# Performance work log

Measured on AMD Instinct MI355X. Metric: run time of the kernel, lower is better.

Reference implementation:

```python
import jax, jax.numpy as jnp
import numpy as np

D_MODEL = 1024
NUM_HEADS = 16
D_HEAD = D_MODEL // NUM_HEADS


def setup_inputs() -> dict:
    key = jax.random.key(0)
    ks = jax.random.split(key, 5)
    b, n = 4, 2048
    x = jax.random.normal(ks[0], (b, n, D_MODEL), dtype=jnp.float32)
    s = 1.0 / np.sqrt(D_MODEL)
    w_qkv = jax.random.normal(ks[1], (D_MODEL, 3 * D_MODEL), dtype=jnp.float32) * s
    b_qkv = jax.random.normal(ks[2], (3 * D_MODEL,), dtype=jnp.float32) * 0.01
    w_out = jax.random.normal(ks[3], (D_MODEL, D_MODEL), dtype=jnp.float32) * s
    b_out = jax.random.normal(ks[4], (D_MODEL,), dtype=jnp.float32) * 0.01
    return {"x": x, "w_qkv": w_qkv, "b_qkv": b_qkv, "w_out": w_out, "b_out": b_out}


def reference(x, w_qkv, b_qkv, w_out, b_out):
    b, n, _ = x.shape
    h, d = NUM_HEADS, D_HEAD
    scale = d ** -0.5
    qkv = x @ w_qkv + b_qkv                       # [b, n, 3*d_model]
    # split as (qkv, h, d) on the feature axis, matching 'b n (qkv h d)'
    qkv = qkv.reshape(b, n, 3, h, d).transpose(2, 0, 3, 1, 4)  # [3, b, h, n, d]
    q, k, v = qkv[0], qkv[1], qkv[2]
    dots = jnp.einsum('bhid,bhjd->bhij', q, k) * scale
    causal = jnp.tril(jnp.ones((n, n), dtype=bool))
    dots = jnp.where(causal[None, None], dots, -jnp.inf)
    attn = jax.nn.softmax(dots, axis=-1)
    out = jnp.einsum('bhij,bhjd->bhid', attn, v)
    out = out.transpose(0, 2, 1, 3).reshape(b, n, h * d)
    return out @ w_out + b_out
```

## Files before the change

### kernel.cpp

```cpp
#include <hip/hip_runtime.h>
#include <hip/hip_bf16.h>
#include <stdint.h>

typedef unsigned short u16;
typedef __attribute__((ext_vector_type(8))) short bf16x8;
typedef __attribute__((ext_vector_type(4))) float f32x4;
typedef __attribute__((ext_vector_type(16))) float f32x16;
typedef __attribute__((ext_vector_type(4))) short s16x4;

#define SEQ   2048
#define BATCH 4

#define MFMA16(a,b,c) __builtin_amdgcn_mfma_f32_16x16x32_bf16(a,b,c,0,0,0)
#define MFMA32(a,b,c) __builtin_amdgcn_mfma_f32_32x32x16_bf16(a,b,c,0,0,0)
#define EXP2F __builtin_amdgcn_exp2f

__device__ __forceinline__ u16 f2bf(float f) {
  union { float f; uint32_t u; } c{f};
  uint32_t r = c.u + 0x7fffu + ((c.u >> 16) & 1u);
  return (u16)(r >> 16);
}

__device__ __forceinline__ void gll16(const void* g, void* l) {
  __builtin_amdgcn_global_load_lds((const __attribute__((address_space(1))) void*)g,
                                   (__attribute__((address_space(3))) void*)l,
                                   16, 0, 0);
}

__global__ __launch_bounds__(256) void k_cvt(const float* __restrict__ in,
                                             u16* __restrict__ out) {
  int i = (blockIdx.x * 256 + threadIdx.x) * 8;
  float4 a = *(const float4*)(in + i);
  float4 b = *(const float4*)(in + i + 4);
  union { u16 u[8]; bf16x8 v; } r;
  r.u[0] = f2bf(a.x); r.u[1] = f2bf(a.y); r.u[2] = f2bf(a.z); r.u[3] = f2bf(a.w);
  r.u[4] = f2bf(b.x); r.u[5] = f2bf(b.y); r.u[6] = f2bf(b.z); r.u[7] = f2bf(b.w);
  *(bf16x8*)(out + i) = r.v;
}

__global__ __launch_bounds__(256) void k_cvtT(const float* __restrict__ in,
                                              u16* __restrict__ out, int K, int N) {
  __shared__ float tl[32][33];
  int tx = threadIdx.x & 31, ty = threadIdx.x >> 5;
  int c0 = blockIdx.x * 32, r0 = blockIdx.y * 32;
#pragma unroll
  for (int j = 0; j < 32; j += 8)
    tl[ty + j][tx] = in[(size_t)(r0 + ty + j) * N + c0 + tx];
  __syncthreads();
#pragma unroll
  for (int j = 0; j < 32; j += 8)
    out[(size_t)(c0 + ty + j) * K + r0 + tx] = f2bf(tl[tx][ty + j]);
}

template<int OUT_BF16>
__global__ __launch_bounds__(256) void k_gemm(const u16* __restrict__ A,
                                              const u16* __restrict__ BT,
                                              const float* __restrict__ bias,
                                              void* __restrict__ Cv, int N, int K) {
  __shared__ alignas(16) u16 As[128 * 32];
  __shared__ alignas(16) u16 Bs[128 * 32];
  const int t = threadIdx.x, l = t & 63, w = t >> 6;
  const int brow = blockIdx.y * 128, bcol = blockIdx.x * 128;
  const int wr = w >> 1, wc = w & 1;
  f32x4 acc[4][4] = {};
  const u16* gA = A + (size_t)(brow + (t >> 2)) * K + (t & 3) * 8;
  const u16* gB = BT + (size_t)(bcol + (t >> 2)) * K + (t & 3) * 8;
  char* lA = (char*)As + w * 1024;
  char* lB = (char*)Bs + w * 1024;
  const int ro = (l & 15) * 64, ko = (l >> 4) * 16;
  for (int k0 = 0; k0 < K; k0 += 32) {
    gll16(gA + k0, lA);
    gll16(gA + (size_t)64 * K + k0, lA + 4096);
    gll16(gB + k0, lB);
    gll16(gB + (size_t)64 * K + k0, lB + 4096);
    __syncthreads();
    bf16x8 af[4], bff[4];
#pragma unroll
    for (int mi = 0; mi < 4; mi++)
      af[mi] = *(const bf16x8*)((const char*)As + (wr * 64 + mi * 16) * 64 + ro + ko);
#pragma unroll
    for (int ni = 0; ni < 4; ni++)
      bff[ni] = *(const bf16x8*)((const char*)Bs + (wc * 64 + ni * 16) * 64 + ro + ko);
#pragma unroll
    for (int mi = 0; mi < 4; mi++)
#pragma unroll
      for (int ni = 0; ni < 4; ni++)
        acc[mi][ni] = MFMA16(af[mi], bff[ni], acc[mi][ni]);
    __syncthreads();
  }
  const int r0 = brow + wr * 64 + (l >> 4) * 4;
  const int c0 = bcol + wc * 64 + (l & 15);
#pragma unroll
  for (int ni = 0; ni < 4; ni++) {
    float bv = bias[c0 + ni * 16];
#pragma unroll
    for (int mi = 0; mi < 4; mi++)
#pragma unroll
      for (int r = 0; r < 4; r++) {
        float v = acc[mi][ni][r] + bv;
        size_t off = (size_t)(r0 + mi * 16 + r) * N + c0 + ni * 16;
        if (OUT_BF16) ((u16*)Cv)[off] = f2bf(v);
        else          ((float*)Cv)[off] = v;
      }
  }
}

#define SBAR  asm volatile("s_barrier" ::: "memory")
#define LGKM0 asm volatile("s_waitcnt lgkmcnt(0)" ::: "memory")
#define VM2   asm volatile("s_waitcnt vmcnt(2)" ::: "memory")
#define VM0   asm volatile("s_waitcnt vmcnt(0)" ::: "memory")

__global__ __launch_bounds__(512, 2) void k_gemm256(const u16* __restrict__ A,
                                                    const u16* __restrict__ BT,
                                                    const float* __restrict__ bias,
                                                    u16* __restrict__ C,
                                                    int N, int K, int NT, int TN) {
  __shared__ alignas(16) char LDS[98304];
  const int t = threadIdx.x;
  const int l = t & 63, w = t >> 6;
  const int wm = w >> 2, wn = w & 3;
  const int lr = l & 15, lg = l >> 4;

  const int nwg = gridDim.x;
  const int cpx = nwg >> 3;
  const int sb = (blockIdx.x & 7) * cpx + (blockIdx.x >> 3);
  const int brow = (sb / TN) * 256, bcol = (sb % TN) * 128;

  auto stageA = [&](int c, int h, int tt) {
#pragma unroll
    for (int i = 0; i < 2; i++) {
      int s = t + i * 512;
      int r = s >> 3, cg = s & 7;
      int grow = brow + (r >> 6) * 128 + h * 64 + (r & 63);
      int gk = tt * 64 + ((cg ^ (r & 7)) * 8);
      gll16(A + (size_t)grow * K + gk, LDS + c * 49152 + h * 16384 + s * 16);
    }
  };
  auto stageB = [&](int c, int tt) {
#pragma unroll
    for (int i = 0; i < 2; i++) {
      int s = t + i * 512;
      int r = s >> 3, cg = s & 7;
      int grow = bcol + r;
      int gk = tt * 64 + ((cg ^ (r & 7)) * 8);
      gll16(BT + (size_t)grow * K + gk, LDS + c * 49152 + 32768 + s * 16);
    }
  };

  f32x4 acc[8][2] = {};
  bf16x8 afr[4], bfr[2];

#define READ_A(c, h, ks)                                                       \
  {                                                                            \
    const char* baseA = LDS + (c) * 49152 + (h) * 16384 + (wm * 64) * 128;     \
    _Pragma("unroll") for (int mi = 0; mi < 4; mi++)                           \
      afr[mi] = *(const bf16x8*)(baseA + (mi * 16 + lr) * 128 +                \
                                 ((((ks) * 4 + lg) ^ (lr & 7)) * 16));         \
  }
#define READ_B(c, ks)                                                          \
  {                                                                            \
    const char* baseB = LDS + (c) * 49152 + 32768 + (wn * 32) * 128;           \
    _Pragma("unroll") for (int ni = 0; ni < 2; ni++)                           \
      bfr[ni] = *(const bf16x8*)(baseB + (ni * 16 + lr) * 128 +                \
                                 ((((ks) * 4 + lg) ^ (lr & 7)) * 16));         \
  }
#define DO_MFMA(H)                                                             \
  {                                                                            \
    __builtin_amdgcn_s_setprio(1);                                             \
    _Pragma("unroll") for (int mi = 0; mi < 4; mi++)                           \
      _Pragma("unroll") for (int ni = 0; ni < 2; ni++)                         \
        acc[(H)*4 + mi][ni] = MFMA16(afr[mi], bfr[ni], acc[(H)*4 + mi][ni]);   \
    __builtin_amdgcn_s_setprio(0);                                             \
  }

  stageA(0, 0, 0);
  stageB(0, 0);
  stageA(0, 1, 0);
  VM2; SBAR;

  for (int tt = 0; tt < NT; tt++) {
    const int c = tt & 1;
    if (tt + 1 < NT) { stageA(c ^ 1, 0, tt + 1); }
    READ_A(c, 0, 0); READ_B(c, 0);
    DO_MFMA(0);
    if (tt + 1 < NT) { VM2; } else { VM0; }
    LGKM0; SBAR;
    if (tt + 1 < NT) { stageB(c ^ 1, tt + 1); }
    READ_A(c, 1, 0);
    DO_MFMA(1);
    LGKM0; SBAR;
    if (tt + 1 < NT) { stageA(c ^ 1, 1, tt + 1); }
    READ_A(c, 1, 1); READ_B(c, 1);
    DO_MFMA(1);
    LGKM0; SBAR;
    READ_A(c, 0, 1);
    DO_MFMA(0);
    VM2;
    LGKM0; SBAR;
  }

  const int r0 = brow + wm * 128 + lg * 4;
  const int c0 = bcol + wn * 32 + lr;
#pragma unroll
  for (int ni = 0; ni < 2; ni++) {
    float bv = bias[c0 + ni * 16];
#pragma unroll
    for (int mig = 0; mig < 8; mig++) {
      const int row = r0 + mig * 16;
#pragma unroll
      for (int r = 0; r < 4; r++)
        C[(size_t)(row + r) * N + c0 + ni * 16] = f2bf(acc[mig][ni][r] + bv);
    }
  }
}
#undef READ_A
#undef READ_B
#undef DO_MFMA

__global__ __launch_bounds__(256) void k_trV(const u16* __restrict__ qkv,
                                             u16* __restrict__ vT) {
  __shared__ u16 s[32][33];
  int tx = threadIdx.x & 31, ty = threadIdx.x >> 5;
  int n0 = blockIdx.x * 32, d0 = blockIdx.y * 32, bh = blockIdx.z;
  int b = bh >> 4, h = bh & 15;
#pragma unroll
  for (int j = 0; j < 32; j += 8)
    s[ty + j][tx] = qkv[(size_t)(b * SEQ + n0 + ty + j) * 3072 + 2048 + h * 64 + d0 + tx];
  __syncthreads();
#pragma unroll
  for (int j = 0; j < 32; j += 8)
    vT[(size_t)(bh * 64 + d0 + ty + j) * SEQ + n0 + tx] = s[tx][ty + j];
}

__global__ __launch_bounds__(256) void k_attn(const u16* __restrict__ qkv,
                                              const u16* __restrict__ vT,
                                              u16* __restrict__ outp) {
  __shared__ alignas(16) char SB[2][16384];
  const int t = threadIdx.x, l = t & 63, w = t >> 6;
  const int hi = l >> 5, q = l & 31;
  const int qp = blockIdx.x, h = blockIdx.y, b = blockIdx.z;
  const int bh = b * 16 + h;
  const int srow = t >> 3;
  const int csw = ((t & 7) * 16) ^ ((srow & 7) << 4);
  const int swz = (q & 7) << 4;
  const float SC = 0.18033688011112042f;

  auto STAGE = [&](char* buf, int kv0) {
    char* lK = buf + w * 1024;
    char* lV = buf + 8192 + w * 1024;
    gll16(qkv + (size_t)(b * SEQ + kv0 + srow) * 3072 + 1024 + h * 64 + (csw >> 1), lK);
    gll16(qkv + (size_t)(b * SEQ + kv0 + srow + 32) * 3072 + 1024 + h * 64 + (csw >> 1), lK + 4096);
    gll16(vT + (size_t)(bh * 64 + srow) * SEQ + kv0 + (csw >> 1), lV);
    gll16(vT + (size_t)(bh * 64 + srow + 32) * SEQ + kv0 + (csw >> 1), lV + 4096);
  };

  for (int tsel = 0; tsel < 2; tsel++) {
    const int qt = tsel ? (15 - qp) : qp;
    const int qr0 = qt * 128 + w * 32;
    const int qg = qr0 + q;
    bf16x8 qf[4];
#pragma unroll
    for (int c = 0; c < 4; c++)
      qf[c] = *(const bf16x8*)(qkv + (size_t)(b * SEQ + qg) * 3072 + h * 64 + c * 16 + hi * 8);
    f32x16 o0 = {}, o1 = {}, lv = {};
    float m_run = -1e30f;
    const int nkv = 2 * qt + 2;

    STAGE(SB[0], 0);
    for (int j = 0; j < nkv; j++) {
      const int kv0 = j * 64;
      __syncthreads();
      if (j + 1 < nkv) STAGE(SB[(j + 1) & 1], kv0 + 64);
      const char* Kb = SB[j & 1];
      const char* Vb = Kb + 8192;

      if (kv0 <= qr0 + 31) {
        f32x16 st0 = {}, st1 = {};
        __builtin_amdgcn_s_setprio(1);
#pragma unroll
        for (int c = 0; c < 4; c++) {
          const int cb = c * 32 + hi * 16;
          bf16x8 k0 = *(const bf16x8*)(Kb + q * 128 + (cb ^ swz));
          bf16x8 k1 = *(const bf16x8*)(Kb + (32 + q) * 128 + (cb ^ swz));
          st0 = MFMA32(k0, qf[c], st0);
          st1 = MFMA32(k1, qf[c], st1);
        }
        __builtin_amdgcn_s_setprio(0);
        if (kv0 + 63 > qr0) {
#pragma unroll
          for (int r = 0; r < 16; r++) {
            const int krow = (r & 3) + 8 * (r >> 2) + 4 * hi;
            if (kv0 + krow > qg)      st0[r] = -1e30f;
            if (kv0 + 32 + krow > qg) st1[r] = -1e30f;
          }
        }
        float tmx[16];
#pragma unroll
        for (int r = 0; r < 16; r++) tmx[r] = fmaxf(st0[r], st1[r]);
        float v0 = fmaxf(fmaxf(tmx[0], tmx[1]), tmx[2]);
        float v1 = fmaxf(fmaxf(tmx[3], tmx[4]), tmx[5]);
        float v2 = fmaxf(fmaxf(tmx[6], tmx[7]), tmx[8]);
        float v3 = fmaxf(fmaxf(tmx[9], tmx[10]), tmx[11]);
        float v4 = fmaxf(fmaxf(tmx[12], tmx[13]), tmx[14]);
        float v5 = fmaxf(fmaxf(v0, v1), tmx[15]);
        float v6 = fmaxf(fmaxf(v2, v3), v4);
        float v7 = fmaxf(v5, v6);
        const float vs = fmaxf(v7, __shfl_xor(v7, 32)) * SC;
        if (__any(vs > m_run + 8.0f)) {
          float mnew = fmaxf(m_run, vs);
          float corr = EXP2F(m_run - mnew);
          m_run = mnew;
#pragma unroll
          for (int r = 0; r < 16; r++) { o0[r] *= corr; o1[r] *= corr; lv[r] *= corr; }
        }
        f32x16 e0 = st0 * SC - m_run;
        f32x16 e1 = st1 * SC - m_run;
        f32x16 p0, p1;
#pragma unroll
        for (int r = 0; r < 16; r++) { p0[r] = EXP2F(e0[r]); p1[r] = EXP2F(e1[r]); }
        lv += p0 + p1;
#pragma unroll
        for (int khb = 0; khb < 2; khb++) {
          uint32_t pk[8], ot[8];
#pragma unroll
          for (int ii = 0; ii < 8; ii++) {
            float lo = khb ? p1[2 * ii] : p0[2 * ii];
            float hf = khb ? p1[2 * ii + 1] : p0[2 * ii + 1];
            asm("v_cvt_pk_bf16_f32 %0, %1, %2" : "=v"(pk[ii]) : "v"(lo), "v"(hf));
          }
#pragma unroll
          for (int ii = 0; ii < 8; ii++) ot[ii] = (uint32_t)__shfl_xor((int)pk[ii], 32);
          union { uint32_t u[4]; bf16x8 v; } be, bo;
          be.u[0] = hi ? ot[2] : pk[0];
          be.u[1] = hi ? ot[3] : pk[1];
          be.u[2] = hi ? pk[2] : ot[0];
          be.u[3] = hi ? pk[3] : ot[1];
          bo.u[0] = hi ? ot[6] : pk[4];
          bo.u[1] = hi ? ot[7] : pk[5];
          bo.u[2] = hi ? pk[6] : ot[4];
          bo.u[3] = hi ? pk[7] : ot[5];
          __builtin_amdgcn_s_setprio(1);
#pragma unroll
          for (int kti = 0; kti < 2; kti++) {
            const int cb = (khb * 2 + kti) * 32 + hi * 16;
            bf16x8 vv0 = *(const bf16x8*)(Vb + q * 128 + (cb ^ swz));
            bf16x8 vv1 = *(const bf16x8*)(Vb + (32 + q) * 128 + (cb ^ swz));
            bf16x8 pb = kti ? bo.v : be.v;
            o0 = MFMA32(vv0, pb, o0);
            o1 = MFMA32(vv1, pb, o1);
          }
          __builtin_amdgcn_s_setprio(0);
        }
      }
    }
    __syncthreads();
    float ls = ((lv[0] + lv[1]) + (lv[2] + lv[3])) + ((lv[4] + lv[5]) + (lv[6] + lv[7]))
             + ((lv[8] + lv[9]) + (lv[10] + lv[11])) + ((lv[12] + lv[13]) + (lv[14] + lv[15]));
    ls += __shfl_xor(ls, 32);
    const float invl = 1.0f / ls;
#pragma unroll
    for (int dh = 0; dh < 2; dh++)
#pragma unroll
      for (int jq = 0; jq < 4; jq++) {
        union { u16 u[4]; s16x4 v; } pk4;
#pragma unroll
        for (int r = 0; r < 4; r++)
          pk4.u[r] = f2bf((dh ? o1[4 * jq + r] : o0[4 * jq + r]) * invl);
        *(s16x4*)(outp + (size_t)(b * SEQ + qg) * 1024 + h * 64 + dh * 32 + jq * 8 + hi * 4) = pk4.v;
      }
  }
}

extern "C" void kernel_launch(void* const* d_in, const int* in_sizes, int n_in,
                              void* d_out, int out_size, void* d_ws, size_t ws_size,
                              hipStream_t stream) {
  const float* x     = (const float*)d_in[0];
  const float* w_qkv = (const float*)d_in[1];
  const float* b_qkv = (const float*)d_in[2];
  const float* w_out = (const float*)d_in[3];
  const float* b_out = (const float*)d_in[4];

  char* ws = (char*)d_ws;
  u16* xbf   = (u16*)(ws);
  u16* wqkvT = (u16*)(ws + (16u << 20));
  u16* woutT = (u16*)(ws + (22u << 20));
  u16* qkvb  = (u16*)(ws + (24u << 20));
  u16* vTb   = (u16*)(ws + (72u << 20));

  k_cvt <<<4096, 256, 0, stream>>>(x, xbf);
  k_cvtT<<<dim3(96, 32), 256, 0, stream>>>(w_qkv, wqkvT, 1024, 3072);
  k_cvtT<<<dim3(32, 32), 256, 0, stream>>>(w_out, woutT, 1024, 1024);
  k_gemm256<<<768, 512, 0, stream>>>(xbf, wqkvT, b_qkv, qkvb, 3072, 1024, 16, 24);
  k_trV <<<dim3(64, 2, 64), 256, 0, stream>>>(qkvb, vTb);
  k_attn<<<dim3(8, 16, 4), 256, 0, stream>>>(qkvb, vTb, xbf);
  k_gemm<0><<<dim3(8, 64), 256, 0, stream>>>(xbf, woutT, b_out, d_out, 1024, 1024);
}
```

Before: 196.7 us.

## Use 256x128 pipelined GEMM for output projection and permlane32 swaps in attention

The output projection now runs on the 256x128 tiled, double-buffered k_gemm256 kernel (templated to write fp32) instead of the simple 128x128 single-stage GEMM. That launch is 256 workgroups of 512 threads, which roughly matches the CU count but leaves little slack for load balance. In the attention kernel, the cross-half shuffles (__shfl_xor by 32) used for the row max, the P-fragment exchange and the final row-sum reduction are replaced with v_permlane32_swap. This removes the LDS-backed bpermute traffic and the per-lane select logic.

Result: faster. 185.7 us (-5.6%).

```diff
diff --git a/kernel.cpp b/kernel.cpp
--- a/kernel.cpp
+++ b/kernel.cpp
@@ -7,6 +7,7 @@
 typedef __attribute__((ext_vector_type(4))) float f32x4;
 typedef __attribute__((ext_vector_type(16))) float f32x16;
 typedef __attribute__((ext_vector_type(4))) short s16x4;
+typedef __attribute__((ext_vector_type(2))) unsigned u32x2;
 
 #define SEQ   2048
 #define BATCH 4
@@ -25,6 +26,23 @@
   __builtin_amdgcn_global_load_lds((const __attribute__((address_space(1))) void*)g,
                                    (__attribute__((address_space(3))) void*)l,
                                    16, 0, 0);
+}
+
+__device__ __forceinline__ void plswap(uint32_t &a, uint32_t &b) {
+  u32x2 r = __builtin_amdgcn_permlane32_swap(a, b, false, false);
+  a = r[0]; b = r[1];
+}
+__device__ __forceinline__ float xhalf_max(float v) {
+  union { float f; uint32_t u; } c{v};
+  u32x2 r = __builtin_amdgcn_permlane32_swap(c.u, c.u, false, false);
+  union { uint32_t u; float f; } x{r[0]}, y{r[1]};
+  return fmaxf(x.f, y.f);
+}
+__device__ __forceinline__ float xhalf_add(float v) {
+  union { float f; uint32_t u; } c{v};
+  u32x2 r = __builtin_amdgcn_permlane32_swap(c.u, c.u, false, false);
+  union { uint32_t u; float f; } x{r[0]}, y{r[1]};
+  return x.f + y.f;
 }
 
 __global__ __launch_bounds__(256) void k_cvt(const float* __restrict__ in,
@@ -52,68 +70,16 @@
     out[(size_t)(c0 + ty + j) * K + r0 + tx] = f2bf(tl[tx][ty + j]);
 }
 
-template<int OUT_BF16>
-__global__ __launch_bounds__(256) void k_gemm(const u16* __restrict__ A,
-                                              const u16* __restrict__ BT,
-                                              const float* __restrict__ bias,
-                                              void* __restrict__ Cv, int N, int K) {
-  __shared__ alignas(16) u16 As[128 * 32];
-  __shared__ alignas(16) u16 Bs[128 * 32];
-  const int t = threadIdx.x, l = t & 63, w = t >> 6;
-  const int brow = blockIdx.y * 128, bcol = blockIdx.x * 128;
-  const int wr = w >> 1, wc = w & 1;
-  f32x4 acc[4][4] = {};
-  const u16* gA = A + (size_t)(brow + (t >> 2)) * K + (t & 3) * 8;
-  const u16* gB = BT + (size_t)(bcol + (t >> 2)) * K + (t & 3) * 8;
-  char* lA = (char*)As + w * 1024;
-  char* lB = (char*)Bs + w * 1024;
-  const int ro = (l & 15) * 64, ko = (l >> 4) * 16;
-  for (int k0 = 0; k0 < K; k0 += 32) {
-    gll16(gA + k0, lA);
-    gll16(gA + (size_t)64 * K + k0, lA + 4096);
-    gll16(gB + k0, lB);
-    gll16(gB + (size_t)64 * K + k0, lB + 4096);
-    __syncthreads();
-    bf16x8 af[4], bff[4];
-#pragma unroll
-    for (int mi = 0; mi < 4; mi++)
-      af[mi] = *(const bf16x8*)((const char*)As + (wr * 64 + mi * 16) * 64 + ro + ko);
-#pragma unroll
-    for (int ni = 0; ni < 4; ni++)
-      bff[ni] = *(const bf16x8*)((const char*)Bs + (wc * 64 + ni * 16) * 64 + ro + ko);
-#pragma unroll
-    for (int mi = 0; mi < 4; mi++)
-#pragma unroll
-      for (int ni = 0; ni < 4; ni++)
-        acc[mi][ni] = MFMA16(af[mi], bff[ni], acc[mi][ni]);
-    __syncthreads();
-  }
-  const int r0 = brow + wr * 64 + (l >> 4) * 4;
-  const int c0 = bcol + wc * 64 + (l & 15);
-#pragma unroll
-  for (int ni = 0; ni < 4; ni++) {
-    float bv = bias[c0 + ni * 16];
-#pragma unroll
-    for (int mi = 0; mi < 4; mi++)
-#pragma unroll
-      for (int r = 0; r < 4; r++) {
-        float v = acc[mi][ni][r] + bv;
-        size_t off = (size_t)(r0 + mi * 16 + r) * N + c0 + ni * 16;
-        if (OUT_BF16) ((u16*)Cv)[off] = f2bf(v);
-        else          ((float*)Cv)[off] = v;
-      }
-  }
-}
-
 #define SBAR  asm volatile("s_barrier" ::: "memory")
 #define LGKM0 asm volatile("s_waitcnt lgkmcnt(0)" ::: "memory")
 #define VM2   asm volatile("s_waitcnt vmcnt(2)" ::: "memory")
 #define VM0   asm volatile("s_waitcnt vmcnt(0)" ::: "memory")
 
+template<int OUT_F32>
 __global__ __launch_bounds__(512, 2) void k_gemm256(const u16* __restrict__ A,
                                                     const u16* __restrict__ BT,
                                                     const float* __restrict__ bias,
-                                                    u16* __restrict__ C,
+                                                    void* __restrict__ Cv,
                                                     int N, int K, int NT, int TN) {
   __shared__ alignas(16) char LDS[98304];
   const int t = threadIdx.x;
@@ -208,8 +174,12 @@
     for (int mig = 0; mig < 8; mig++) {
       const int row = r0 + mig * 16;
 #pragma unroll
-      for (int r = 0; r < 4; r++)
-        C[(size_t)(row + r) * N + c0 + ni * 16] = f2bf(acc[mig][ni][r] + bv);
+      for (int r = 0; r < 4; r++) {
+        float v = acc[mig][ni][r] + bv;
+        size_t off = (size_t)(row + r) * N + c0 + ni * 16;
+        if (OUT_F32) ((float*)Cv)[off] = v;
+        else         ((u16*)Cv)[off]   = f2bf(v);
+      }
     }
   }
 }
@@ -305,7 +275,7 @@
         float v5 = fmaxf(fmaxf(v0, v1), tmx[15]);
         float v6 = fmaxf(fmaxf(v2, v3), v4);
         float v7 = fmaxf(v5, v6);
-        const float vs = fmaxf(v7, __shfl_xor(v7, 32)) * SC;
+        const float vs = xhalf_max(v7) * SC;
         if (__any(vs > m_run + 8.0f)) {
           float mnew = fmaxf(m_run, vs);
           float corr = EXP2F(m_run - mnew);
@@ -321,24 +291,18 @@
         lv += p0 + p1;
 #pragma unroll
         for (int khb = 0; khb < 2; khb++) {
-          uint32_t pk[8], ot[8];
+          uint32_t pk[8];
 #pragma unroll
           for (int ii = 0; ii < 8; ii++) {
             float lo = khb ? p1[2 * ii] : p0[2 * ii];
             float hf = khb ? p1[2 * ii + 1] : p0[2 * ii + 1];
             asm("v_cvt_pk_bf16_f32 %0, %1, %2" : "=v"(pk[ii]) : "v"(lo), "v"(hf));
           }
-#pragma unroll
-          for (int ii = 0; ii < 8; ii++) ot[ii] = (uint32_t)__shfl_xor((int)pk[ii], 32);
+          plswap(pk[0], pk[2]); plswap(pk[1], pk[3]);
+          plswap(pk[4], pk[6]); plswap(pk[5], pk[7]);
           union { uint32_t u[4]; bf16x8 v; } be, bo;
-          be.u[0] = hi ? ot[2] : pk[0];
-          be.u[1] = hi ? ot[3] : pk[1];
-          be.u[2] = hi ? pk[2] : ot[0];
-          be.u[3] = hi ? pk[3] : ot[1];
-          bo.u[0] = hi ? ot[6] : pk[4];
-          bo.u[1] = hi ? ot[7] : pk[5];
-          bo.u[2] = hi ? pk[6] : ot[4];
-          bo.u[3] = hi ? pk[7] : ot[5];
+          be.u[0] = pk[0]; be.u[1] = pk[1]; be.u[2] = pk[2]; be.u[3] = pk[3];
+          bo.u[0] = pk[4]; bo.u[1] = pk[5]; bo.u[2] = pk[6]; bo.u[3] = pk[7];
           __builtin_amdgcn_s_setprio(1);
 #pragma unroll
           for (int kti = 0; kti < 2; kti++) {
@@ -356,7 +320,7 @@
     __syncthreads();
     float ls = ((lv[0] + lv[1]) + (lv[2] + lv[3])) + ((lv[4] + lv[5]) + (lv[6] + lv[7]))
              + ((lv[8] + lv[9]) + (lv[10] + lv[11])) + ((lv[12] + lv[13]) + (lv[14] + lv[15]));
-    ls += __shfl_xor(ls, 32);
+    ls = xhalf_add(ls);
     const float invl = 1.0f / ls;
 #pragma unroll
     for (int dh = 0; dh < 2; dh++)
@@ -390,8 +354,8 @@
   k_cvt <<<4096, 256, 0, stream>>>(x, xbf);
   k_cvtT<<<dim3(96, 32), 256, 0, stream>>>(w_qkv, wqkvT, 1024, 3072);
   k_cvtT<<<dim3(32, 32), 256, 0, stream>>>(w_out, woutT, 1024, 1024);
-  k_gemm256<<<768, 512, 0, stream>>>(xbf, wqkvT, b_qkv, qkvb, 3072, 1024, 16, 24);
+  k_gemm256<0><<<768, 512, 0, stream>>>(xbf, wqkvT, b_qkv, qkvb, 3072, 1024, 16, 24);
   k_trV <<<dim3(64, 2, 64), 256, 0, stream>>>(qkvb, vTb);
   k_attn<<<dim3(8, 16, 4), 256, 0, stream>>>(qkvb, vTb, xbf);
-  k_gemm<0><<<dim3(8, 64), 256, 0, stream>>>(xbf, woutT, b_out, d_out, 1024, 1024);
-}
+  k_gemm256<1><<<256, 512, 0, stream>>>(xbf, woutT, b_out, d_out, 1024, 1024, 16, 8);
+}
```
